# Optimization experiments

Measured on AMD Instinct MI355X. Metric: run time of the kernel, lower is better.

The kernel has to match this reference:

```python
import jax, jax.numpy as jnp
import numpy as np

B, S, D, H = 2, 2048, 1024, 16
DK = D // H

def setup_inputs() -> dict:
    key = jax.random.key(0)
    ks = jax.random.split(key, 11)
    scale = 1.0 / np.sqrt(D)
    inp = {
        'q': jax.random.normal(ks[0], (B, S, D), jnp.float32),
        'k': jax.random.normal(ks[1], (B, S, D), jnp.float32),
        'v': jax.random.normal(ks[2], (B, S, D), jnp.float32),
        'Wq': jax.random.normal(ks[3], (D, D), jnp.float32) * scale,
        'bq': jnp.zeros((D,), jnp.float32),
        'Wk': jax.random.normal(ks[4], (D, D), jnp.float32) * scale,
        'bk': jnp.zeros((D,), jnp.float32),
        'Wv': jax.random.normal(ks[5], (D, D), jnp.float32) * scale,
        'bv': jnp.zeros((D,), jnp.float32),
        'Wo': jax.random.normal(ks[6], (D, D), jnp.float32) * scale,
        'bo': jnp.zeros((D,), jnp.float32),
    }
    return inp

def reference(q, k, v, Wq, bq, Wk, bk, Wv, bv, Wo, bo):
    # linear projections
    qp = q @ Wq + bq   # [B,S,D]
    kp = k @ Wk + bk
    vp = v @ Wv + bv
    # split heads -> [B,H,S,DK]
    qh = qp.reshape(B, S, H, DK).transpose(0, 2, 1, 3)
    kh = kp.reshape(B, S, H, DK).transpose(0, 2, 1, 3)
    vh = vp.reshape(B, S, H, DK).transpose(0, 2, 1, 3)
    scaled = jnp.einsum('bhqd,bhkd->bhqk', qh, kh) / jnp.sqrt(jnp.float32(DK))
    attn_score = jax.nn.softmax(scaled, axis=-1)  # [B,H,S,S]
    x = jnp.einsum('bhqk,bhkd->bhqd', attn_score, vh)
    # dropout is identity in eval mode
    out = x.transpose(0, 2, 1, 3).reshape(B, S, D)
    return (out @ Wo + bo, attn_score)
```

## Files before the change

kernel.cpp:

```cpp
#include <hip/hip_runtime.h>
#include <hip/hip_bf16.h>
#include <stdint.h>
#include <stddef.h>

typedef unsigned short u16;
typedef __attribute__((ext_vector_type(8))) short short8;
typedef __attribute__((ext_vector_type(4))) short bfx4;
typedef __attribute__((ext_vector_type(4))) float f32x4;
typedef __attribute__((ext_vector_type(4))) float f4;

constexpr int B_ = 2, S_ = 2048, D_ = 1024, H_ = 16;
constexpr size_t OUT_ELEMS = (size_t)B_ * S_ * D_;

__device__ __forceinline__ u16 f2bf(float f) {
    union { float f; unsigned u; } v; v.f = f;
    unsigned r = 0x7FFFu + ((v.u >> 16) & 1u);
    return (u16)((v.u + r) >> 16);
}

__device__ __forceinline__ unsigned cvtpk(float lo, float hi) {
    unsigned r;
    asm("v_cvt_pk_bf16_f32 %0, %1, %2" : "=v"(r) : "v"(lo), "v"(hi));
    return r;
}

__device__ __forceinline__ void gload16(const void* g, void* l) {
    auto gg = reinterpret_cast<const __attribute__((address_space(1))) unsigned*>(
        reinterpret_cast<uintptr_t>(g));
    auto ll = reinterpret_cast<__attribute__((address_space(3))) unsigned*>(
        reinterpret_cast<uintptr_t>(l));
    __builtin_amdgcn_global_load_lds(gg, ll, 16, 0, 0);
}

#define VMWAIT(N) do { asm volatile("s_waitcnt vmcnt(" #N ")" ::: "memory"); } while (0)
#define LGKMWAIT0() do { asm volatile("s_waitcnt lgkmcnt(0)" ::: "memory"); } while (0)
__device__ __forceinline__ void barrier_() {
    __builtin_amdgcn_s_barrier();
    __builtin_amdgcn_sched_barrier(0);
}

__global__ __launch_bounds__(256) void wtrans_kernel(
    const float* __restrict__ W0, const float* __restrict__ W1,
    const float* __restrict__ W2, const float* __restrict__ W3,
    u16* __restrict__ T0, u16* __restrict__ T1, u16* __restrict__ T2, u16* __restrict__ T3)
{
    __shared__ __align__(16) u16 Ts[64][72];
    const float* W = blockIdx.z == 0 ? W0 : blockIdx.z == 1 ? W1 : blockIdx.z == 2 ? W2 : W3;
    u16*         T = blockIdx.z == 0 ? T0 : blockIdx.z == 1 ? T1 : blockIdx.z == 2 ? T2 : T3;
    const int t = threadIdx.x;
    const int r0 = blockIdx.y * 64, c0 = blockIdx.x * 64;
    const int row = t >> 2, qd = t & 3;

    const float* src = W + (size_t)(r0 + row) * 1024 + c0 + qd * 16;
    u16 tmp[16];
    #pragma unroll
    for (int j = 0; j < 16; j += 4) {
        f4 v = *(const f4*)(src + j);
        tmp[j] = f2bf(v[0]); tmp[j+1] = f2bf(v[1]); tmp[j+2] = f2bf(v[2]); tmp[j+3] = f2bf(v[3]);
    }
    #pragma unroll
    for (int j = 0; j < 16; j++) Ts[row][qd * 16 + j] = tmp[j];
    __syncthreads();
    short8 o0, o1;
    #pragma unroll
    for (int j = 0; j < 8; j++) { o0[j] = (short)Ts[qd*16 + j][row]; o1[j] = (short)Ts[qd*16 + 8 + j][row]; }
    u16* dst = T + (size_t)(c0 + row) * 1024 + r0 + qd * 16;
    *(short8*)dst = o0;
    *(short8*)(dst + 8) = o1;
}

__global__ __launch_bounds__(256) void vtrans_kernel(const u16* __restrict__ vp, u16* __restrict__ vt)
{
    __shared__ __align__(16) u16 Vs[64][72];
    const int t = threadIdx.x;
    const int s0 = blockIdx.x * 64;
    const int bh = blockIdx.y, b = bh >> 4, h = bh & 15;
    #pragma unroll
    for (int i = 0; i < 2; i++) {
        int c = t + 256 * i, row = c >> 3, ch = c & 7;
        *(short8*)(&Vs[row][ch * 8]) =
            *(const short8*)(vp + ((size_t)b * S_ + s0 + row) * D_ + h * 64 + ch * 8);
    }
    __syncthreads();
    #pragma unroll
    for (int i = 0; i < 2; i++) {
        int c = t + 256 * i, d = c >> 3, ch = c & 7;
        short8 o;
        #pragma unroll
        for (int j = 0; j < 8; j++) o[j] = (short)Vs[ch * 8 + j][d];
        *(short8*)(vt + ((size_t)bh * 64 + d) * S_ + s0 + ch * 8) = o;
    }
}

struct StageF { f4 v[4]; };

__device__ __forceinline__ void a_load(StageF& st, const float* Af, int row0, int k0, int t) {
    const int row = t >> 1, half = t & 1;
    const float* p = Af + (size_t)(row0 + row) * D_ + k0 + half * 16;
    st.v[0] = *(const f4*)(p);
    st.v[1] = *(const f4*)(p + 4);
    st.v[2] = *(const f4*)(p + 8);
    st.v[3] = *(const f4*)(p + 12);
}

__device__ __forceinline__ void a_store(const StageF& st, u16* Ls, int t) {
    const int row = t >> 1, half = t & 1;
    union { unsigned u[4]; short8 s8; } h0, h1;
    h0.u[0] = cvtpk(st.v[0][0], st.v[0][1]); h0.u[1] = cvtpk(st.v[0][2], st.v[0][3]);
    h0.u[2] = cvtpk(st.v[1][0], st.v[1][1]); h0.u[3] = cvtpk(st.v[1][2], st.v[1][3]);
    h1.u[0] = cvtpk(st.v[2][0], st.v[2][1]); h1.u[1] = cvtpk(st.v[2][2], st.v[2][3]);
    h1.u[2] = cvtpk(st.v[3][0], st.v[3][1]); h1.u[3] = cvtpk(st.v[3][2], st.v[3][3]);
    const int sw = (row & 3) << 4;
    *(short8*)((char*)Ls + row * 64 + ((half * 32) ^ sw))      = h0.s8;
    *(short8*)((char*)Ls + row * 64 + ((half * 32 + 16) ^ sw)) = h1.s8;
}

__global__ __launch_bounds__(256, 3)
void gemm_qkvf(const float* __restrict__ A0, const float* __restrict__ A1, const float* __restrict__ A2,
               const u16* __restrict__ Bt0, const u16* __restrict__ Bt1, const u16* __restrict__ Bt2,
               const float* __restrict__ bi0, const float* __restrict__ bi1, const float* __restrict__ bi2,
               u16* __restrict__ Cq, u16* __restrict__ Ck, u16* __restrict__ Cv)
{
    constexpr int K = D_, N = D_;
    __shared__ __align__(16) u16 As[2][128 * 32];
    __shared__ __align__(16) u16 Bs[2][128 * 32];

    const int z = blockIdx.z;
    const float* Aptr = z == 0 ? A0  : z == 1 ? A1  : A2;
    const u16*   Bt   = z == 0 ? Bt0 : z == 1 ? Bt1 : Bt2;
    const float* bias = z == 0 ? bi0 : z == 1 ? bi1 : bi2;
    u16*         Cptr = z == 0 ? Cq  : z == 1 ? Ck  : Cv;
    const float scale = z == 0 ? 0.125f : 1.0f;

    const int t = threadIdx.x;
    const int w = t >> 6, l = t & 63, lr = l >> 4, lc = l & 15;
    const int wr = w >> 1, wc = w & 1;
    const int id = blockIdx.y * 8 + blockIdx.x;
    const int xcd = id & 7, i_ = id >> 3;
    const int row0 = ((xcd << 2) | ((i_ >> 4) << 1) | ((i_ >> 3) & 1)) * 128;
    const int col0 = (i_ & 7) * 128;
    const int NI = K >> 5;

    auto issueB = [&](int i, u16* dst) {
        #pragma unroll
        for (int j = 0; j < 2; j++) {
            int off = j * 256 + t;
            int row = off >> 2, ch = off & 3;
            const char* src = (const char*)Bt + (((size_t)(col0 + row) * K + i * 32) << 1)
                              + ((ch ^ (row & 3)) << 4);
            gload16(src, (char*)dst + off * 16);
        }
    };

    f32x4 acc[4][4] = {};
    StageF sa;
    issueB(0, Bs[0]);
    a_load(sa, Aptr, row0, 0, t);

    for (int i = 0; i < NI; i++) {
        const int p = i & 1;
        a_store(sa, As[p], t);
        LGKMWAIT0();
        barrier_();
        if (i + 1 < NI) {
            issueB(i + 1, Bs[p ^ 1]);
            a_load(sa, Aptr, row0, (i + 1) * 32, t);
        }

        short8 af[4], bf_[4];
        #pragma unroll
        for (int mm = 0; mm < 4; mm++) {
            int r = wr * 64 + mm * 16 + lc;
            af[mm] = *(const short8*)((const char*)As[p] + r * 64 + ((lr * 16) ^ ((r & 3) << 4)));
        }
        #pragma unroll
        for (int nn = 0; nn < 4; nn++) {
            int r = wc * 64 + nn * 16 + lc;
            bf_[nn] = *(const short8*)((const char*)Bs[p] + r * 64 + ((lr * 16) ^ ((r & 3) << 4)));
        }
        #pragma unroll
        for (int mm = 0; mm < 4; mm++)
            #pragma unroll
            for (int nn = 0; nn < 4; nn++)
                acc[mm][nn] = __builtin_amdgcn_mfma_f32_16x16x32_bf16(af[mm], bf_[nn], acc[mm][nn], 0, 0, 0);
    }

    float bv[4];
    #pragma unroll
    for (int nn = 0; nn < 4; nn++) bv[nn] = bias[col0 + wc * 64 + nn * 16 + lc];

    #pragma unroll
    for (int mm = 0; mm < 4; mm++) {
        const int row = row0 + wr * 64 + mm * 16 + lr * 4;
        #pragma unroll
        for (int nn = 0; nn < 4; nn++) {
            const int col = col0 + wc * 64 + nn * 16 + lc;
            #pragma unroll
            for (int r = 0; r < 4; r++)
                Cptr[(size_t)(row + r) * N + col] = f2bf((acc[mm][nn][r] + bv[nn]) * scale);
        }
    }
}

__global__ __launch_bounds__(256, 3)
void gemm_out(const u16* __restrict__ Aptr, const u16* __restrict__ Bt,
              const float* __restrict__ bias, float* __restrict__ Cptr)
{
    constexpr int K = D_, N = D_;
    __shared__ __align__(16) u16 As[2][128 * 32];
    __shared__ __align__(16) u16 Bs[2][128 * 32];

    const int t = threadIdx.x;
    const int w = t >> 6, l = t & 63, lr = l >> 4, lc = l & 15;
    const int wr = w >> 1, wc = w & 1;
    const int id = blockIdx.y * 8 + blockIdx.x;
    const int xcd = id & 7, i_ = id >> 3;
    const int row0 = ((xcd << 2) | ((i_ >> 4) << 1) | ((i_ >> 3) & 1)) * 128;
    const int col0 = (i_ & 7) * 128;
    const int NI = K >> 5;

    auto issueT = [&](const u16* P, int r0_, int i, u16* dst) {
        #pragma unroll
        for (int j = 0; j < 2; j++) {
            int off = j * 256 + t;
            int row = off >> 2, ch = off & 3;
            const char* src = (const char*)P + (((size_t)(r0_ + row) * K + i * 32) << 1)
                              + ((ch ^ (row & 3)) << 4);
            gload16(src, (char*)dst + off * 16);
        }
    };

    f32x4 acc[4][4] = {};
    issueT(Bt, col0, 0, Bs[0]);
    issueT(Aptr, row0, 0, As[0]);

    for (int i = 0; i < NI; i++) {
        const int p = i & 1;
        if (i + 1 < NI) {
            issueT(Bt, col0, i + 1, Bs[p ^ 1]);
            issueT(Aptr, row0, i + 1, As[p ^ 1]);
            VMWAIT(4);
        } else {
            VMWAIT(0);
        }
        barrier_();

        short8 af[4], bf_[4];
        #pragma unroll
        for (int mm = 0; mm < 4; mm++) {
            int r = wr * 64 + mm * 16 + lc;
            af[mm] = *(const short8*)((const char*)As[p] + r * 64 + ((lr * 16) ^ ((r & 3) << 4)));
        }
        #pragma unroll
        for (int nn = 0; nn < 4; nn++) {
            int r = wc * 64 + nn * 16 + lc;
            bf_[nn] = *(const short8*)((const char*)Bs[p] + r * 64 + ((lr * 16) ^ ((r & 3) << 4)));
        }
        #pragma unroll
        for (int mm = 0; mm < 4; mm++)
            #pragma unroll
            for (int nn = 0; nn < 4; nn++)
                acc[mm][nn] = __builtin_amdgcn_mfma_f32_16x16x32_bf16(af[mm], bf_[nn], acc[mm][nn], 0, 0, 0);
        __builtin_amdgcn_s_barrier();
    }

    float bv[4];
    #pragma unroll
    for (int nn = 0; nn < 4; nn++) bv[nn] = bias[col0 + wc * 64 + nn * 16 + lc];

    #pragma unroll
    for (int mm = 0; mm < 4; mm++) {
        const int row = row0 + wr * 64 + mm * 16 + lr * 4;
        #pragma unroll
        for (int nn = 0; nn < 4; nn++) {
            const int col = col0 + wc * 64 + nn * 16 + lc;
            #pragma unroll
            for (int r = 0; r < 4; r++)
                Cptr[(size_t)(row + r) * N + col] = acc[mm][nn][r] + bv[nn];
        }
    }
}

__global__ __launch_bounds__(512, 4)
void attn_kernel(const u16* __restrict__ qp, const u16* __restrict__ kp,
                 const u16* __restrict__ vt, float* __restrict__ Pout,
                 u16* __restrict__ xout)
{
    __shared__ __align__(16) u16 Ks[2][128 * 64];
    __shared__ __align__(16) u16 Vts[2][64 * 128];
    __shared__ __align__(16) float Pls[8][16][32];

    const int t = threadIdx.x;
    const int w = t >> 6, l = t & 63, lr = l >> 4, lc = l & 15;
    const int bid = blockIdx.x;
    const int s = ((bid & 7) << 6) | (bid >> 3);
    const int q0 = (s & 15) * 128;
    const int bh = s >> 4, b = bh >> 4, h = bh & 15;
    const float L2E = 1.4426950408889634f;
    constexpr int NT = S_ / 128;

    auto issueK = [&](int kt, int buf) {
        #pragma unroll
        for (int i = 0; i < 2; i++) {
            int off = i * 512 + t, row = off >> 3, ch = off & 7;
            const char* src = (const char*)kp + ((((size_t)b * S_ + kt * 128 + row) * D_ + h * 64) << 1)
                              + ((ch ^ (row & 7)) << 4);
            gload16(src, (char*)Ks[buf] + off * 16);
        }
    };
    auto issueV = [&](int kt, int buf) {
        #pragma unroll
        for (int i = 0; i < 2; i++) {
            int off = i * 512 + t, row = off >> 4, ch = off & 15;
            const char* src = (const char*)vt + ((((size_t)bh * 64 + row) * S_ + kt * 128) << 1)
                              + ((ch ^ (row & 7)) << 4);
            gload16(src, (char*)Vts[buf] + off * 16);
        }
    };

    issueK(0, 0);
    short8 qf[2];
    {
        const u16* qrow = qp + ((size_t)b * S_ + q0 + w * 16 + lc) * D_ + h * 64;
        qf[0] = *(const short8*)(qrow + lr * 8);
        qf[1] = *(const short8*)(qrow + 32 + lr * 8);
    }

    float sum = 0.f;
    for (int kt = 0; kt < NT; kt++) {
        const int p = kt & 1;
        if (kt + 1 < NT) { issueK(kt + 1, p ^ 1); VMWAIT(2); }
        else             { VMWAIT(0); }
        barrier_();
        const char* Kb = (const char*)Ks[p];
        #pragma unroll
        for (int f = 0; f < 8; f++) {
            int r = f * 16 + lc, sw = (r & 7) << 4;
            const char* kb = Kb + r * 128;
            short8 k0 = *(const short8*)(kb + ((lr * 16) ^ sw));
            short8 k1 = *(const short8*)(kb + ((64 + lr * 16) ^ sw));
            f32x4 sacc = {};
            sacc = __builtin_amdgcn_mfma_f32_16x16x32_bf16(k0, qf[0], sacc, 0, 0, 0);
            sacc = __builtin_amdgcn_mfma_f32_16x16x32_bf16(k1, qf[1], sacc, 0, 0, 0);
            sum += exp2f(sacc[0] * L2E) + exp2f(sacc[1] * L2E)
                 + exp2f(sacc[2] * L2E) + exp2f(sacc[3] * L2E);
        }
        __builtin_amdgcn_s_barrier();
    }
    issueK(0, 0); issueV(0, 0);
    sum += __shfl_xor(sum, 16);
    sum += __shfl_xor(sum, 32);
    const float l2i = -log2f(sum);

    f32x4 xacc[4] = {};
    float* pls = &Pls[w][0][0];
    float* prow0 = Pout + ((size_t)bh * S_ + q0 + w * 16) * S_;

    for (int kt = 0; kt < NT; kt++) {
        const int p = kt & 1;
        if (kt + 1 < NT) { issueK(kt + 1, p ^ 1); issueV(kt + 1, p ^ 1); }
        if (kt == 0)           VMWAIT(4);
        else if (kt + 1 < NT)  VMWAIT(12);
        else                   VMWAIT(8);
        barrier_();
        const char* Kb = (const char*)Ks[p];
        const char* Vb = (const char*)Vts[p];

        #pragma unroll
        for (int kk = 0; kk < 4; kk++) {
            union { unsigned u[4]; short8 s8; } pu;
            #pragma unroll
            for (int fo = 0; fo < 2; fo++) {
                const int f = kk * 2 + fo;
                int r = f * 16 + lc, sw = (r & 7) << 4;
                const char* kb = Kb + r * 128;
                short8 k0 = *(const short8*)(kb + ((lr * 16) ^ sw));
                short8 k1 = *(const short8*)(kb + ((64 + lr * 16) ^ sw));
                f32x4 sacc = {};
                __builtin_amdgcn_s_setprio(1);
                sacc = __builtin_amdgcn_mfma_f32_16x16x32_bf16(k0, qf[0], sacc, 0, 0, 0);
                sacc = __builtin_amdgcn_mfma_f32_16x16x32_bf16(k1, qf[1], sacc, 0, 0, 0);
                __builtin_amdgcn_s_setprio(0);
                f32x4 pv_;
                pv_[0] = exp2f(fmaf(sacc[0], L2E, l2i));
                pv_[1] = exp2f(fmaf(sacc[1], L2E, l2i));
                pv_[2] = exp2f(fmaf(sacc[2], L2E, l2i));
                pv_[3] = exp2f(fmaf(sacc[3], L2E, l2i));
                *(f32x4*)((char*)pls + lc * 128 + (((fo * 64 + lr * 16)) ^ ((lc & 7) << 4))) = pv_;
                pu.u[fo * 2 + 0] = cvtpk(pv_[0], pv_[1]);
                pu.u[fo * 2 + 1] = cvtpk(pv_[2], pv_[3]);
            }
            {
                float* prow = prow0 + (size_t)kt * 128 + kk * 32;
                #pragma unroll
                for (int half = 0; half < 2; half++) {
                    int row = half * 8 + (l >> 3), chunk = l & 7;
                    f32x4 pr = *(const f32x4*)((const char*)pls + row * 128
                               + ((chunk * 16) ^ (((l >> 3) & 7) << 4)));
                    *(f32x4*)(prow + (size_t)row * S_ + chunk * 4) = pr;
                }
            }
            const short8 pa = pu.s8;
            __builtin_amdgcn_s_setprio(1);
            #pragma unroll
            for (int n = 0; n < 4; n++) {
                int rr = n * 16 + lc, sw2 = (rr & 7) << 4;
                const char* vrow = Vb + rr * 256;
                union { bfx4 h[2]; short8 s8; } vu;
                vu.h[0] = *(const bfx4*)(vrow + ((kk * 64 + lr * 8) ^ sw2));
                vu.h[1] = *(const bfx4*)(vrow + ((kk * 64 + 32 + lr * 8) ^ sw2));
                xacc[n] = __builtin_amdgcn_mfma_f32_16x16x32_bf16(pa, vu.s8, xacc[n], 0, 0, 0);
            }
            __builtin_amdgcn_s_setprio(0);
        }
        __builtin_amdgcn_s_barrier();
    }

    #pragma unroll
    for (int n = 0; n < 4; n++) {
        #pragma unroll
        for (int r = 0; r < 4; r++) {
            int row = q0 + w * 16 + lr * 4 + r;
            int col = h * 64 + n * 16 + lc;
            xout[((size_t)b * S_ + row) * D_ + col] = f2bf(xacc[n][r]);
        }
    }
}

extern "C" void kernel_launch(void* const* d_in, const int* in_sizes, int n_in,
                              void* d_out, int out_size, void* d_ws, size_t ws_size,
                              hipStream_t stream)
{
    const float* qin = (const float*)d_in[0];
    const float* kin = (const float*)d_in[1];
    const float* vin = (const float*)d_in[2];
    const float* Wq  = (const float*)d_in[3];
    const float* bq  = (const float*)d_in[4];
    const float* Wk  = (const float*)d_in[5];
    const float* bk  = (const float*)d_in[6];
    const float* Wv  = (const float*)d_in[7];
    const float* bv  = (const float*)d_in[8];
    const float* Wo  = (const float*)d_in[9];
    const float* bo  = (const float*)d_in[10];

    u16* base = (u16*)d_ws;
    u16* Wqt = base;
    u16* Wkt = base + 1048576;
    u16* Wvt = base + 2097152;
    u16* Wot = base + 3145728;
    u16* qpb = base + 4194304;
    u16* kpb = base + 8388608;
    u16* vpb = base + 12582912;
    u16* vtb = base + 16777216;
    u16* xb  = base + 20971520;

    float* out  = (float*)d_out;
    float* Pout = out + OUT_ELEMS;

    wtrans_kernel<<<dim3(16, 16, 4), 256, 0, stream>>>(Wq, Wk, Wv, Wo, Wqt, Wkt, Wvt, Wot);
    gemm_qkvf<<<dim3(8, 32, 3), 256, 0, stream>>>(
        qin, kin, vin, Wqt, Wkt, Wvt, bq, bk, bv, qpb, kpb, vpb);
    vtrans_kernel<<<dim3(32, 32), 256, 0, stream>>>(vpb, vtb);
    attn_kernel<<<512, 512, 0, stream>>>(qpb, kpb, vtb, Pout, xb);
    gemm_out<<<dim3(8, 32), 256, 0, stream>>>(xb, Wot, bo, out);
}
```

Measured before the change: 258.8 us.

## Split softmax denominator pass across waves by key range instead of LDS-staged tiles

The first attention pass, which computes softmax row sums, no longer streams K tiles through double-buffered shared memory with barriers. Each of the 8 waves now takes a 256-key slice, loads K fragments straight from global memory, and computes partial sums for all 128 query rows of the block, holding all Q fragments in registers. The partials are reduced through shared memory with one __syncthreads. This removes per-tile barriers and LDS traffic and lets the first K/V tile prefetch for the second pass overlap the sum pass. The cost is higher register pressure and uncoalesced direct global K loads.

```diff
diff --git a/kernel.cpp b/kernel.cpp
--- a/kernel.cpp
+++ b/kernel.cpp
@@ -318,38 +318,50 @@
         }
     };
 
-    issueK(0, 0);
     short8 qf[2];
     {
         const u16* qrow = qp + ((size_t)b * S_ + q0 + w * 16 + lc) * D_ + h * 64;
         qf[0] = *(const short8*)(qrow + lr * 8);
         qf[1] = *(const short8*)(qrow + 32 + lr * 8);
     }
-
+    issueK(0, 0); issueV(0, 0);
+
+    short8 qf1[8][2];
+    #pragma unroll
+    for (int qb = 0; qb < 8; qb++) {
+        const u16* qrow = qp + ((size_t)b * S_ + q0 + qb * 16 + lc) * D_ + h * 64;
+        qf1[qb][0] = *(const short8*)(qrow + lr * 8);
+        qf1[qb][1] = *(const short8*)(qrow + 32 + lr * 8);
+    }
+    float psum[8] = {0.f, 0.f, 0.f, 0.f, 0.f, 0.f, 0.f, 0.f};
+    #pragma unroll 2
+    for (int kb = 0; kb < 16; kb++) {
+        const u16* krow = kp + ((size_t)b * S_ + w * 256 + kb * 16 + lc) * D_ + h * 64;
+        short8 kf0 = *(const short8*)(krow + lr * 8);
+        short8 kf1 = *(const short8*)(krow + 32 + lr * 8);
+        #pragma unroll
+        for (int qb = 0; qb < 8; qb++) {
+            f32x4 sacc = {};
+            sacc = __builtin_amdgcn_mfma_f32_16x16x32_bf16(kf0, qf1[qb][0], sacc, 0, 0, 0);
+            sacc = __builtin_amdgcn_mfma_f32_16x16x32_bf16(kf1, qf1[qb][1], sacc, 0, 0, 0);
+            psum[qb] += exp2f(sacc[0] * L2E) + exp2f(sacc[1] * L2E)
+                      + exp2f(sacc[2] * L2E) + exp2f(sacc[3] * L2E);
+        }
+    }
+    #pragma unroll
+    for (int qb = 0; qb < 8; qb++) {
+        psum[qb] += __shfl_xor(psum[qb], 16);
+        psum[qb] += __shfl_xor(psum[qb], 32);
+    }
+    float* Psum = &Pls[0][0][0];
+    if (l < 16) {
+        #pragma unroll
+        for (int qb = 0; qb < 8; qb++) Psum[(w * 8 + qb) * 16 + lc] = psum[qb];
+    }
+    __syncthreads();
     float sum = 0.f;
-    for (int kt = 0; kt < NT; kt++) {
-        const int p = kt & 1;
-        if (kt + 1 < NT) { issueK(kt + 1, p ^ 1); VMWAIT(2); }
-        else             { VMWAIT(0); }
-        barrier_();
-        const char* Kb = (const char*)Ks[p];
-        #pragma unroll
-        for (int f = 0; f < 8; f++) {
-            int r = f * 16 + lc, sw = (r & 7) << 4;
-            const char* kb = Kb + r * 128;
-            short8 k0 = *(const short8*)(kb + ((lr * 16) ^ sw));
-            short8 k1 = *(const short8*)(kb + ((64 + lr * 16) ^ sw));
-            f32x4 sacc = {};
-            sacc = __builtin_amdgcn_mfma_f32_16x16x32_bf16(k0, qf[0], sacc, 0, 0, 0);
-            sacc = __builtin_amdgcn_mfma_f32_16x16x32_bf16(k1, qf[1], sacc, 0, 0, 0);
-            sum += exp2f(sacc[0] * L2E) + exp2f(sacc[1] * L2E)
-                 + exp2f(sacc[2] * L2E) + exp2f(sacc[3] * L2E);
-        }
-        __builtin_amdgcn_s_barrier();
-    }
-    issueK(0, 0); issueV(0, 0);
-    sum += __shfl_xor(sum, 16);
-    sum += __shfl_xor(sum, 32);
+    #pragma unroll
+    for (int wp = 0; wp < 8; wp++) sum += Psum[(wp * 8 + w) * 16 + lc];
     const float l2i = -log2f(sum);
 
     f32x4 xacc[4] = {};
```

Measured after the change: 266.2 us. 2.9% more time.
